# Optimization experiments

Measured on AMD Instinct MI355X. Metric: run time of the kernel, lower is better.

Reference implementation:

```python
import jax, jax.numpy as jnp
import numpy as np

D_MODEL = 1024
NUM_HEADS = 16
D_K = D_MODEL // NUM_HEADS
LN_EPS = 1e-5


def setup_inputs() -> dict:
    key = jax.random.key(0)
    ks = jax.random.split(key, 9)
    s = 1.0 / np.sqrt(D_MODEL)
    x = jax.random.normal(ks[0], (4, 2048, D_MODEL), dtype=jnp.float32)
    Wq = jax.random.uniform(ks[1], (D_MODEL, D_MODEL), minval=-s, maxval=s, dtype=jnp.float32)
    bq = jax.random.uniform(ks[2], (D_MODEL,), minval=-s, maxval=s, dtype=jnp.float32)
    Wk = jax.random.uniform(ks[3], (D_MODEL, D_MODEL), minval=-s, maxval=s, dtype=jnp.float32)
    bk = jax.random.uniform(ks[4], (D_MODEL,), minval=-s, maxval=s, dtype=jnp.float32)
    Wv = jax.random.uniform(ks[5], (D_MODEL, D_MODEL), minval=-s, maxval=s, dtype=jnp.float32)
    bv = jax.random.uniform(ks[6], (D_MODEL,), minval=-s, maxval=s, dtype=jnp.float32)
    Wo = jax.random.uniform(ks[7], (D_MODEL, D_MODEL), minval=-s, maxval=s, dtype=jnp.float32)
    bo = jax.random.uniform(ks[8], (D_MODEL,), minval=-s, maxval=s, dtype=jnp.float32)
    gamma = jnp.ones((D_MODEL,), dtype=jnp.float32)
    beta = jnp.zeros((D_MODEL,), dtype=jnp.float32)
    return {"x": x, "Wq": Wq, "bq": bq, "Wk": Wk, "bk": bk, "Wv": Wv, "bv": bv,
            "Wo": Wo, "bo": bo, "gamma": gamma, "beta": beta}


def reference(x, Wq, bq, Wk, bk, Wv, bv, Wo, bo, gamma, beta):
    B, S, D = x.shape
    H, dk = NUM_HEADS, D_K
    # torch Linear: y = x @ W^T + b; split heads -> (B, H, S, dk)
    def proj(W, b):
        return (jnp.einsum('bsd,ed->bse', x, W) + b).reshape(B, S, H, dk).transpose(0, 2, 1, 3)
    Q = proj(Wq, bq)
    K = proj(Wk, bk)
    V = proj(Wv, bv)
    scores = jnp.einsum('bhqd,bhkd->bhqk', Q, K) / jnp.sqrt(jnp.float32(dk))
    attn = jax.nn.softmax(scores, axis=-1)  # dropout is identity in eval mode
    ctx = jnp.einsum('bhqk,bhkd->bhqd', attn, V)
    ctx = ctx.transpose(0, 2, 1, 3).reshape(B, S, D)
    out = jnp.einsum('bsd,ed->bse', ctx, Wo) + bo
    y = out + x
    mu = jnp.mean(y, axis=-1, keepdims=True)
    var = jnp.mean(jnp.square(y - mu), axis=-1, keepdims=True)
    return (y - mu) * jax.lax.rsqrt(var + LN_EPS) * gamma + beta
```

## Files before the change

### kernel.cpp

```cpp
#include <hip/hip_runtime.h>


#define SEQ 2048
#define DMODEL 1024
#define NH 16
#define DK 64
#define NROWS 8192

typedef unsigned short u16;
typedef unsigned int u32;
typedef __bf16 bf16;
typedef bf16 bf16x8 __attribute__((ext_vector_type(8)));
typedef float f32x4 __attribute__((ext_vector_type(4)));
typedef float f32x16 __attribute__((ext_vector_type(16)));
typedef unsigned u32x2 __attribute__((ext_vector_type(2)));

__device__ inline u16 bfbits(float f) { return __builtin_bit_cast(u16, (bf16)f); }
__device__ inline u32 packbf2(float a, float b) {
    return (u32)bfbits(a) | ((u32)bfbits(b) << 16);
}

__device__ inline float sexp2(float s) {
    return __builtin_bit_cast(float, (u32)(int)fmaf(s, 8388608.0f, 1064986823.0f));
}

__device__ inline void gload16(const u16* g, u16* l) {
    __builtin_amdgcn_global_load_lds(
        (const __attribute__((address_space(1))) u32*)g,
        (__attribute__((address_space(3))) u32*)l, 16, 0, 0);
}

__device__ inline void plswap(u32& a, u32& b) {
#if __has_builtin(__builtin_amdgcn_permlane32_swap)
    u32x2 r = __builtin_amdgcn_permlane32_swap(a, b, false, false);
    a = r[0]; b = r[1];
#else
    u32 xa = __shfl_xor(a, 32), xb = __shfl_xor(b, 32);
    int hi = (threadIdx.x & 63) >> 5;
    u32 na = hi ? xb : a;
    u32 nb = hi ? b : xa;
    a = na; b = nb;
#endif
}

__global__ __launch_bounds__(256) void cvt_f32_bf16(const float* __restrict__ in,
                                                    u16* __restrict__ out, int n) {
    int i = (blockIdx.x * 256 + threadIdx.x) * 4;
    if (i >= n) return;
    float4 v = *(const float4*)(in + i);
    ushort4 o;
    o.x = bfbits(v.x); o.y = bfbits(v.y); o.z = bfbits(v.z); o.w = bfbits(v.w);
    *(ushort4*)(out + i) = o;
}

__global__ __launch_bounds__(256) void cvt4_w(const float* __restrict__ w0,
                                              const float* __restrict__ w1,
                                              const float* __restrict__ w2,
                                              const float* __restrict__ w3,
                                              u16* __restrict__ o0, u16* __restrict__ o1,
                                              u16* __restrict__ o2, u16* __restrict__ o3) {
    const float* in;
    u16* out;
    switch (blockIdx.y) {
        case 0: in = w0; out = o0; break;
        case 1: in = w1; out = o1; break;
        case 2: in = w2; out = o2; break;
        default: in = w3; out = o3; break;
    }
    int i = (blockIdx.x * 256 + threadIdx.x) * 4;
    float4 v = *(const float4*)(in + i);
    ushort4 o;
    o.x = bfbits(v.x); o.y = bfbits(v.y); o.z = bfbits(v.z); o.w = bfbits(v.w);
    *(ushort4*)(out + i) = o;
}

template <int EPI>
__global__ __launch_bounds__(256) void gemm_bt(
    const u16* __restrict__ A, const u16* __restrict__ Bm,
    const float* __restrict__ bias0, const float* __restrict__ bias1,
    const float* __restrict__ bias2,
    u16* __restrict__ Qo, u16* __restrict__ Ko, u16* __restrict__ Vo,
    const float* __restrict__ xres, float* __restrict__ yout) {
    __shared__ __align__(16) u16 smem[16384];
    u16* As = smem;
    u16* Bs = smem + 8192;

    const int tid  = threadIdx.x;
    const int lane = tid & 63;
    const int w    = tid >> 6;
    const int wr   = (w >> 1) * 64;
    const int wc   = (w & 1) * 64;
    const int l16  = lane & 15;
    const int lq   = lane >> 4;
    const int m0   = blockIdx.x * 128;
    const int n0   = blockIdx.y * 128;

    f32x4 acc[4][4];
#pragma unroll
    for (int m = 0; m < 4; m++)
#pragma unroll
        for (int n = 0; n < 4; n++) {
            f32x4 z = {0.f, 0.f, 0.f, 0.f};
            acc[m][n] = z;
        }

    const int l8r = lane >> 3;
    const int sch = (lane & 7) ^ l8r;
    const u16* a_g = A  + (size_t)(m0 + w * 32 + l8r) * 1024 + sch * 8;
    const u16* b_g = Bm + (size_t)(n0 + w * 32 + l8r) * 1024 + sch * 8;

    for (int k0 = 0; k0 < 1024; k0 += 64) {
        __syncthreads();
#pragma unroll
        for (int i = 0; i < 4; i++) {
            gload16(a_g + (size_t)i * 8192 + k0, As + (w * 32 + i * 8) * 64);
            gload16(b_g + (size_t)i * 8192 + k0, Bs + (w * 32 + i * 8) * 64);
        }
        __syncthreads();

#pragma unroll
        for (int kk = 0; kk < 2; kk++) {
            bf16x8 af[4], bfr[4];
#pragma unroll
            for (int m = 0; m < 4; m++)
                af[m] = *(const bf16x8*)&As[(wr + m * 16 + l16) * 64 +
                                            (((kk << 2) | lq) ^ (l16 & 7)) * 8];
#pragma unroll
            for (int n = 0; n < 4; n++)
                bfr[n] = *(const bf16x8*)&Bs[(wc + n * 16 + l16) * 64 +
                                             (((kk << 2) | lq) ^ (l16 & 7)) * 8];
            __builtin_amdgcn_s_setprio(1);
#pragma unroll
            for (int m = 0; m < 4; m++)
#pragma unroll
                for (int n = 0; n < 4; n++)
                    acc[m][n] = __builtin_amdgcn_mfma_f32_16x16x32_bf16(
                        af[m], bfr[n], acc[m][n], 0, 0, 0);
            __builtin_amdgcn_s_setprio(0);
        }
    }

    if (EPI == 0 && n0 >= 2048) {
        const int e0 = n0 - 2048;
        __syncthreads();
#pragma unroll
        for (int m = 0; m < 4; m++)
#pragma unroll
            for (int n = 0; n < 4; n++) {
                const int col = wc + n * 16 + l16;
                const int row = wr + lq * 4 + m * 16;
                const float bias = bias2[e0 + col];
                ushort4 pk;
                pk.x = bfbits(acc[m][n][0] + bias);
                pk.y = bfbits(acc[m][n][1] + bias);
                pk.z = bfbits(acc[m][n][2] + bias);
                pk.w = bfbits(acc[m][n][3] + bias);
                *(ushort4*)&smem[col * 128 + (row ^ ((col & 7) << 3))] = pk;
            }
        __syncthreads();
        const int b = m0 >> 11;
        const int sbase = m0 & 2047;
#pragma unroll
        for (int i = 0; i < 8; i++) {
            const int c = tid + 256 * i;
            const int col = c >> 4;
            const int s0 = (c & 15) * 8;
            uint4 val = *(const uint4*)&smem[col * 128 + (s0 ^ ((col & 7) << 3))];
            const int eg = e0 + col;
            const int bh = b * NH + (eg >> 6);
            *(uint4*)&Vo[((size_t)bh * DK + (eg & 63)) * SEQ + sbase + s0] = val;
        }
        return;
    }

    const int rbase = m0 + wr + lq * 4;
    const int cbase = n0 + wc + l16;
#pragma unroll
    for (int m = 0; m < 4; m++)
#pragma unroll
        for (int n = 0; n < 4; n++) {
            const int col = cbase + n * 16;
#pragma unroll
            for (int r = 0; r < 4; r++) {
                const int row = rbase + m * 16 + r;
                float v = acc[m][n][r];
                if (EPI == 0) {
                    const int which = col >> 10;
                    const int e = col & 1023;
                    v += (which == 0) ? bias0[e] : bias1[e];
                    if (which == 0) v *= 0.18033688011112042f;
                    const int h = e >> 6, d = e & 63;
                    const int b = row >> 11, s = row & 2047;
                    const int bh = b * NH + h;
                    if (which == 0)
                        Qo[((size_t)bh * SEQ + s) * DK + d] = bfbits(v);
                    else
                        Ko[((size_t)bh * SEQ + s) * DK + d] = bfbits(v);
                } else {
                    v += bias0[col] + xres[(size_t)row * DMODEL + col];
                    yout[(size_t)row * DMODEL + col] = v;
                }
            }
        }
}

__global__ __launch_bounds__(512) void attn(const u16* __restrict__ Qb,
                                            const u16* __restrict__ Kb,
                                            const u16* __restrict__ Vtb,
                                            u16* __restrict__ ctx) {
    __shared__ __align__(16) u16 smem[16384];

    const int tid  = threadIdx.x;
    const int lane = tid & 63;
    const int w    = tid >> 6;
    const int q    = lane & 31;
    const int hi   = lane >> 5;
    const int bh   = blockIdx.x;
    const int q0   = blockIdx.y * 256 + w * 32;

    const u16* qp = Qb + ((size_t)bh * SEQ + q0 + q) * DK + hi * 8;
    bf16x8 qf0 = *(const bf16x8*)(qp);
    bf16x8 qf1 = *(const bf16x8*)(qp + 16);
    bf16x8 qf2 = *(const bf16x8*)(qp + 32);
    bf16x8 qf3 = *(const bf16x8*)(qp + 48);

    const int l8r = lane >> 3;
    const int sch = (lane & 7) ^ l8r;
    const u16* kg = Kb  + ((size_t)bh * SEQ + w * 8 + l8r) * 64 + sch * 8;
    const u16* vg = Vtb + ((size_t)bh * DK  + w * 8 + l8r) * SEQ + sch * 8;
    u16* kl = smem + w * 512;
    u16* vl = smem + 8192 + w * 512;

    f32x16 oacc0, oacc1;
#pragma unroll
    for (int r = 0; r < 16; r++) { oacc0[r] = 0.f; oacc1[r] = 0.f; }
    f32x16 fzero;
#pragma unroll
    for (int r = 0; r < 16; r++) fzero[r] = 0.f;
    float l_ = 0.f;

    gload16(kg, kl);
    gload16(vg, vl);
    __syncthreads();

    for (int t = 0; t < SEQ / 64; t++) {
        if (t < SEQ / 64 - 1) {
            gload16(kg + (size_t)(t + 1) * 4096, kl + ((t + 1) & 1) * 4096);
            gload16(vg + (size_t)(t + 1) * 64,  vl + ((t + 1) & 1) * 4096);
        }
        const u16* Kl = smem + (t & 1) * 4096;
        const u16* Vl = smem + 8192 + (t & 1) * 4096;

        f32x16 sacc0, sacc1;
        {
            bf16x8 k00 = *(const bf16x8*)&Kl[(q)      * 64 + ((0 | hi) ^ (q & 7)) * 8];
            bf16x8 k01 = *(const bf16x8*)&Kl[(q)      * 64 + ((2 | hi) ^ (q & 7)) * 8];
            bf16x8 k02 = *(const bf16x8*)&Kl[(q)      * 64 + ((4 | hi) ^ (q & 7)) * 8];
            bf16x8 k03 = *(const bf16x8*)&Kl[(q)      * 64 + ((6 | hi) ^ (q & 7)) * 8];
            bf16x8 k10 = *(const bf16x8*)&Kl[(q + 32) * 64 + ((0 | hi) ^ (q & 7)) * 8];
            bf16x8 k11 = *(const bf16x8*)&Kl[(q + 32) * 64 + ((2 | hi) ^ (q & 7)) * 8];
            bf16x8 k12 = *(const bf16x8*)&Kl[(q + 32) * 64 + ((4 | hi) ^ (q & 7)) * 8];
            bf16x8 k13 = *(const bf16x8*)&Kl[(q + 32) * 64 + ((6 | hi) ^ (q & 7)) * 8];
            __builtin_amdgcn_s_setprio(1);
            sacc0 = __builtin_amdgcn_mfma_f32_32x32x16_bf16(k00, qf0, fzero, 0, 0, 0);
            sacc1 = __builtin_amdgcn_mfma_f32_32x32x16_bf16(k10, qf0, fzero, 0, 0, 0);
            sacc0 = __builtin_amdgcn_mfma_f32_32x32x16_bf16(k01, qf1, sacc0, 0, 0, 0);
            sacc1 = __builtin_amdgcn_mfma_f32_32x32x16_bf16(k11, qf1, sacc1, 0, 0, 0);
            sacc0 = __builtin_amdgcn_mfma_f32_32x32x16_bf16(k02, qf2, sacc0, 0, 0, 0);
            sacc1 = __builtin_amdgcn_mfma_f32_32x32x16_bf16(k12, qf2, sacc1, 0, 0, 0);
            sacc0 = __builtin_amdgcn_mfma_f32_32x32x16_bf16(k03, qf3, sacc0, 0, 0, 0);
            sacc1 = __builtin_amdgcn_mfma_f32_32x32x16_bf16(k13, qf3, sacc1, 0, 0, 0);
            __builtin_amdgcn_s_setprio(0);
        }

#pragma unroll
        for (int r = 0; r < 16; r++) sacc0[r] = sexp2(sacc0[r]);
#pragma unroll
        for (int r = 0; r < 16; r++) sacc1[r] = sexp2(sacc1[r]);
        {
            float s0 = ((sacc0[0] + sacc0[1]) + (sacc0[2] + sacc0[3])) +
                       ((sacc0[4] + sacc0[5]) + (sacc0[6] + sacc0[7]));
            float s1 = ((sacc0[8] + sacc0[9]) + (sacc0[10] + sacc0[11])) +
                       ((sacc0[12] + sacc0[13]) + (sacc0[14] + sacc0[15]));
            float s2 = ((sacc1[0] + sacc1[1]) + (sacc1[2] + sacc1[3])) +
                       ((sacc1[4] + sacc1[5]) + (sacc1[6] + sacc1[7]));
            float s3 = ((sacc1[8] + sacc1[9]) + (sacc1[10] + sacc1[11])) +
                       ((sacc1[12] + sacc1[13]) + (sacc1[14] + sacc1[15]));
            l_ += (s0 + s1) + (s2 + s3);
        }

        u32 wa[8], wb[8];
#pragma unroll
        for (int i = 0; i < 8; i++) wa[i] = packbf2(sacc0[2 * i], sacc0[2 * i + 1]);
#pragma unroll
        for (int i = 0; i < 8; i++) wb[i] = packbf2(sacc1[2 * i], sacc1[2 * i + 1]);
        plswap(wa[0], wa[2]); plswap(wa[1], wa[3]);
        plswap(wa[4], wa[6]); plswap(wa[5], wa[7]);
        plswap(wb[0], wb[2]); plswap(wb[1], wb[3]);
        plswap(wb[4], wb[6]); plswap(wb[5], wb[7]);
        union { u32 u[4]; bf16x8 v; } pf0, pf1, pf2, pf3;
        pf0.u[0] = wa[0]; pf0.u[1] = wa[1]; pf0.u[2] = wa[2]; pf0.u[3] = wa[3];
        pf1.u[0] = wa[4]; pf1.u[1] = wa[5]; pf1.u[2] = wa[6]; pf1.u[3] = wa[7];
        pf2.u[0] = wb[0]; pf2.u[1] = wb[1]; pf2.u[2] = wb[2]; pf2.u[3] = wb[3];
        pf3.u[0] = wb[4]; pf3.u[1] = wb[5]; pf3.u[2] = wb[6]; pf3.u[3] = wb[7];

        {
            bf16x8 v00 = *(const bf16x8*)&Vl[(q)      * 64 + ((0 | hi) ^ (q & 7)) * 8];
            bf16x8 v01 = *(const bf16x8*)&Vl[(q)      * 64 + ((2 | hi) ^ (q & 7)) * 8];
            bf16x8 v02 = *(const bf16x8*)&Vl[(q)      * 64 + ((4 | hi) ^ (q & 7)) * 8];
            bf16x8 v03 = *(const bf16x8*)&Vl[(q)      * 64 + ((6 | hi) ^ (q & 7)) * 8];
            bf16x8 v10 = *(const bf16x8*)&Vl[(q + 32) * 64 + ((0 | hi) ^ (q & 7)) * 8];
            bf16x8 v11 = *(const bf16x8*)&Vl[(q + 32) * 64 + ((2 | hi) ^ (q & 7)) * 8];
            bf16x8 v12 = *(const bf16x8*)&Vl[(q + 32) * 64 + ((4 | hi) ^ (q & 7)) * 8];
            bf16x8 v13 = *(const bf16x8*)&Vl[(q + 32) * 64 + ((6 | hi) ^ (q & 7)) * 8];
            __builtin_amdgcn_s_setprio(1);
            oacc0 = __builtin_amdgcn_mfma_f32_32x32x16_bf16(v00, pf0.v, oacc0, 0, 0, 0);
            oacc1 = __builtin_amdgcn_mfma_f32_32x32x16_bf16(v10, pf0.v, oacc1, 0, 0, 0);
            oacc0 = __builtin_amdgcn_mfma_f32_32x32x16_bf16(v01, pf1.v, oacc0, 0, 0, 0);
            oacc1 = __builtin_amdgcn_mfma_f32_32x32x16_bf16(v11, pf1.v, oacc1, 0, 0, 0);
            oacc0 = __builtin_amdgcn_mfma_f32_32x32x16_bf16(v02, pf2.v, oacc0, 0, 0, 0);
            oacc1 = __builtin_amdgcn_mfma_f32_32x32x16_bf16(v12, pf2.v, oacc1, 0, 0, 0);
            oacc0 = __builtin_amdgcn_mfma_f32_32x32x16_bf16(v03, pf3.v, oacc0, 0, 0, 0);
            oacc1 = __builtin_amdgcn_mfma_f32_32x32x16_bf16(v13, pf3.v, oacc1, 0, 0, 0);
            __builtin_amdgcn_s_setprio(0);
        }

        __syncthreads();
    }

    const float lfull = l_ + __shfl_xor(l_, 32);
    const float invl = 1.f / lfull;
    const int wbase = w * 2048;
#pragma unroll
    for (int r = 0; r < 16; r++) {
        const int dk0 = (r & 3) + 8 * (r >> 2) + 4 * hi;
        const int dk1 = 32 + dk0;
        smem[wbase + q * 64 + (((dk0 >> 3) ^ (q & 7)) << 3) + (dk0 & 7)] = bfbits(oacc0[r] * invl);
        smem[wbase + q * 64 + (((dk1 >> 3) ^ (q & 7)) << 3) + (dk1 & 7)] = bfbits(oacc1[r] * invl);
    }
    __syncthreads();
    const int b = bh >> 4, h = bh & 15;
    const int r4 = lane >> 1;
    const int cc = (lane & 1) * 4;
#pragma unroll
    for (int c = 0; c < 4; c++) {
        const int chunk = cc + c;
        uint4 val = *(const uint4*)&smem[wbase + r4 * 64 + ((chunk ^ (r4 & 7)) << 3)];
        *(uint4*)&ctx[((size_t)(b * SEQ + q0 + r4)) * DMODEL + h * DK + chunk * 8] = val;
    }
}

__global__ __launch_bounds__(256) void ln_inplace(float* __restrict__ y,
                                                  const float* __restrict__ gamma,
                                                  const float* __restrict__ beta) {
    const int row = blockIdx.x;
    float* p = y + (size_t)row * DMODEL;
    const int tid = threadIdx.x;
    float4 v = *(const float4*)(p + tid * 4);
    float s  = v.x + v.y + v.z + v.w;
    float sq = v.x * v.x + v.y * v.y + v.z * v.z + v.w * v.w;
#pragma unroll
    for (int m = 1; m < 64; m <<= 1) {
        s  += __shfl_xor(s, m);
        sq += __shfl_xor(sq, m);
    }
    __shared__ float rs[4], rq[4];
    if ((tid & 63) == 0) { rs[tid >> 6] = s; rq[tid >> 6] = sq; }
    __syncthreads();
    s  = rs[0] + rs[1] + rs[2] + rs[3];
    sq = rq[0] + rq[1] + rq[2] + rq[3];
    const float mean = s * (1.0f / 1024.0f);
    const float var  = sq * (1.0f / 1024.0f) - mean * mean;
    const float inv  = rsqrtf(var + 1e-5f);
    const int c = tid * 4;
    float4 g4 = *(const float4*)(gamma + c);
    float4 b4 = *(const float4*)(beta + c);
    float4 o;
    o.x = (v.x - mean) * inv * g4.x + b4.x;
    o.y = (v.y - mean) * inv * g4.y + b4.y;
    o.z = (v.z - mean) * inv * g4.z + b4.z;
    o.w = (v.w - mean) * inv * g4.w + b4.w;
    *(float4*)(p + c) = o;
}

extern "C" void kernel_launch(void* const* d_in, const int* in_sizes, int n_in,
                              void* d_out, int out_size, void* d_ws, size_t ws_size,
                              hipStream_t stream) {
    const float* x     = (const float*)d_in[0];
    const float* Wq    = (const float*)d_in[1];
    const float* bq    = (const float*)d_in[2];
    const float* Wk    = (const float*)d_in[3];
    const float* bk    = (const float*)d_in[4];
    const float* Wv    = (const float*)d_in[5];
    const float* bv    = (const float*)d_in[6];
    const float* Wo    = (const float*)d_in[7];
    const float* bo    = (const float*)d_in[8];
    const float* gamma = (const float*)d_in[9];
    const float* beta  = (const float*)d_in[10];
    float* out = (float*)d_out;

    u16* x_bf    = (u16*)d_ws;
    u16* Wqkv_bf = x_bf + (size_t)NROWS * DMODEL;
    u16* Wo_bf   = Wqkv_bf + (size_t)3072 * 1024;
    u16* Q_bf    = Wo_bf + (size_t)1024 * 1024;
    u16* K_bf    = Q_bf + (size_t)64 * SEQ * DK;
    u16* Vt_bf   = K_bf + (size_t)64 * SEQ * DK;
    u16* ctx_bf  = x_bf;

    cvt_f32_bf16<<<8192, 256, 0, stream>>>(x, x_bf, NROWS * DMODEL);
    cvt4_w<<<dim3(1024, 4), 256, 0, stream>>>(Wq, Wk, Wv, Wo,
                                              Wqkv_bf, Wqkv_bf + 1048576,
                                              Wqkv_bf + 2097152, Wo_bf);

    gemm_bt<0><<<dim3(64, 24), 256, 0, stream>>>(x_bf, Wqkv_bf,
                                                 bq, bk, bv, Q_bf, K_bf, Vt_bf,
                                                 nullptr, nullptr);
    attn<<<dim3(64, 8), 512, 0, stream>>>(Q_bf, K_bf, Vt_bf, ctx_bf);
    gemm_bt<1><<<dim3(64, 8), 256, 0, stream>>>(ctx_bf, Wo_bf,
                                                bo, nullptr, nullptr,
                                                nullptr, nullptr, nullptr,
                                                x, out);
    ln_inplace<<<8192, 256, 0, stream>>>(out, gamma, beta);
}
```

Baseline: 204.6 us.

## Split attention over two key halves and add a combine kernel

```diff
diff --git a/kernel.cpp b/kernel.cpp
--- a/kernel.cpp
+++ b/kernel.cpp
@@ -18,6 +18,9 @@
 __device__ inline u16 bfbits(float f) { return __builtin_bit_cast(u16, (bf16)f); }
 __device__ inline u32 packbf2(float a, float b) {
     return (u32)bfbits(a) | ((u32)bfbits(b) << 16);
+}
+__device__ inline float bf2f(u16 h) {
+    union { u32 u; float f; } v; v.u = (u32)h << 16; return v.f;
 }
 
 __device__ inline float sexp2(float s) {
@@ -207,7 +210,8 @@
 __global__ __launch_bounds__(512) void attn(const u16* __restrict__ Qb,
                                             const u16* __restrict__ Kb,
                                             const u16* __restrict__ Vtb,
-                                            u16* __restrict__ ctx) {
+                                            u16* __restrict__ pO,
+                                            float* __restrict__ lG) {
     __shared__ __align__(16) u16 smem[16384];
 
     const int tid  = threadIdx.x;
@@ -216,6 +220,7 @@
     const int q    = lane & 31;
     const int hi   = lane >> 5;
     const int bh   = blockIdx.x;
+    const int ks   = blockIdx.z;
     const int q0   = blockIdx.y * 256 + w * 32;
 
     const u16* qp = Qb + ((size_t)bh * SEQ + q0 + q) * DK + hi * 8;
@@ -226,8 +231,8 @@
 
     const int l8r = lane >> 3;
     const int sch = (lane & 7) ^ l8r;
-    const u16* kg = Kb  + ((size_t)bh * SEQ + w * 8 + l8r) * 64 + sch * 8;
-    const u16* vg = Vtb + ((size_t)bh * DK  + w * 8 + l8r) * SEQ + sch * 8;
+    const u16* kg = Kb  + ((size_t)bh * SEQ + ks * 1024 + w * 8 + l8r) * 64 + sch * 8;
+    const u16* vg = Vtb + ((size_t)bh * DK + w * 8 + l8r) * SEQ + ks * 1024 + sch * 8;
     u16* kl = smem + w * 512;
     u16* vl = smem + 8192 + w * 512;
 
@@ -243,8 +248,8 @@
     gload16(vg, vl);
     __syncthreads();
 
-    for (int t = 0; t < SEQ / 64; t++) {
-        if (t < SEQ / 64 - 1) {
+    for (int t = 0; t < 16; t++) {
+        if (t < 15) {
             gload16(kg + (size_t)(t + 1) * 4096, kl + ((t + 1) & 1) * 4096);
             gload16(vg + (size_t)(t + 1) * 64,  vl + ((t + 1) & 1) * 4096);
         }
@@ -328,26 +333,44 @@
         __syncthreads();
     }
 
-    const float lfull = l_ + __shfl_xor(l_, 32);
-    const float invl = 1.f / lfull;
+    l_ = l_ + __shfl_xor(l_, 32);
+    if (lane < 32) lG[((size_t)(ks * 64 + bh)) * SEQ + q0 + lane] = l_;
+
     const int wbase = w * 2048;
 #pragma unroll
     for (int r = 0; r < 16; r++) {
         const int dk0 = (r & 3) + 8 * (r >> 2) + 4 * hi;
         const int dk1 = 32 + dk0;
-        smem[wbase + q * 64 + (((dk0 >> 3) ^ (q & 7)) << 3) + (dk0 & 7)] = bfbits(oacc0[r] * invl);
-        smem[wbase + q * 64 + (((dk1 >> 3) ^ (q & 7)) << 3) + (dk1 & 7)] = bfbits(oacc1[r] * invl);
+        smem[wbase + q * 64 + (((dk0 >> 3) ^ (q & 7)) << 3) + (dk0 & 7)] = bfbits(oacc0[r]);
+        smem[wbase + q * 64 + (((dk1 >> 3) ^ (q & 7)) << 3) + (dk1 & 7)] = bfbits(oacc1[r]);
     }
     __syncthreads();
-    const int b = bh >> 4, h = bh & 15;
     const int r4 = lane >> 1;
     const int cc = (lane & 1) * 4;
 #pragma unroll
     for (int c = 0; c < 4; c++) {
         const int chunk = cc + c;
         uint4 val = *(const uint4*)&smem[wbase + r4 * 64 + ((chunk ^ (r4 & 7)) << 3)];
-        *(uint4*)&ctx[((size_t)(b * SEQ + q0 + r4)) * DMODEL + h * DK + chunk * 8] = val;
-    }
+        *(uint4*)&pO[(((size_t)(ks * 64 + bh)) * SEQ + q0 + r4) * DK + chunk * 8] = val;
+    }
+}
+
+__global__ __launch_bounds__(256) void combine(const u16* __restrict__ pO,
+                                               const float* __restrict__ lG,
+                                               u16* __restrict__ ctx) {
+    const int t = blockIdx.x * 256 + threadIdx.x;
+    const int chunk = t & 7;
+    const int s = (t >> 3) & 2047;
+    const int bh = t >> 14;
+    const float inv = 1.f / (lG[(size_t)bh * SEQ + s] + lG[(size_t)(64 + bh) * SEQ + s]);
+    union { uint4 v; u16 h[8]; } a, b, o;
+    a.v = *(const uint4*)&pO[((size_t)bh * SEQ + s) * DK + chunk * 8];
+    b.v = *(const uint4*)&pO[((size_t)(64 + bh) * SEQ + s) * DK + chunk * 8];
+#pragma unroll
+    for (int i = 0; i < 8; i++)
+        o.h[i] = bfbits((bf2f(a.h[i]) + bf2f(b.h[i])) * inv);
+    const int bb = bh >> 4, h = bh & 15;
+    *(uint4*)&ctx[((size_t)(bb * SEQ + s)) * DMODEL + h * DK + chunk * 8] = o.v;
 }
 
 __global__ __launch_bounds__(256) void ln_inplace(float* __restrict__ y,
@@ -406,6 +429,8 @@
     u16* K_bf    = Q_bf + (size_t)64 * SEQ * DK;
     u16* Vt_bf   = K_bf + (size_t)64 * SEQ * DK;
     u16* ctx_bf  = x_bf;
+    u16* pO      = (u16*)d_out;
+    float* lG    = (float*)Wqkv_bf;
 
     cvt_f32_bf16<<<8192, 256, 0, stream>>>(x, x_bf, NROWS * DMODEL);
     cvt4_w<<<dim3(1024, 4), 256, 0, stream>>>(Wq, Wk, Wv, Wo,
@@ -415,7 +440,8 @@
     gemm_bt<0><<<dim3(64, 24), 256, 0, stream>>>(x_bf, Wqkv_bf,
                                                  bq, bk, bv, Q_bf, K_bf, Vt_bf,
                                                  nullptr, nullptr);
-    attn<<<dim3(64, 8), 512, 0, stream>>>(Q_bf, K_bf, Vt_bf, ctx_bf);
+    attn<<<dim3(64, 8, 2), 512, 0, stream>>>(Q_bf, K_bf, Vt_bf, pO, lG);
+    combine<<<4096, 256, 0, stream>>>(pO, lG, ctx_bf);
     gemm_bt<1><<<dim3(64, 8), 256, 0, stream>>>(ctx_bf, Wo_bf,
                                                 bo, nullptr, nullptr,
                                                 nullptr, nullptr, nullptr,
```

After: 217.0 us. 1.06x slower.

## Merge conversion kernels and split attention tile loop to cut register pressure

Applied to the files above, without the earlier changes.

```diff
diff --git a/kernel.cpp b/kernel.cpp
--- a/kernel.cpp
+++ b/kernel.cpp
@@ -43,31 +43,29 @@
 #endif
 }
 
-__global__ __launch_bounds__(256) void cvt_f32_bf16(const float* __restrict__ in,
-                                                    u16* __restrict__ out, int n) {
-    int i = (blockIdx.x * 256 + threadIdx.x) * 4;
-    if (i >= n) return;
-    float4 v = *(const float4*)(in + i);
-    ushort4 o;
-    o.x = bfbits(v.x); o.y = bfbits(v.y); o.z = bfbits(v.z); o.w = bfbits(v.w);
-    *(ushort4*)(out + i) = o;
-}
-
-__global__ __launch_bounds__(256) void cvt4_w(const float* __restrict__ w0,
-                                              const float* __restrict__ w1,
-                                              const float* __restrict__ w2,
-                                              const float* __restrict__ w3,
-                                              u16* __restrict__ o0, u16* __restrict__ o1,
-                                              u16* __restrict__ o2, u16* __restrict__ o3) {
+__global__ __launch_bounds__(256) void cvt_all(
+    const float* __restrict__ x,  const float* __restrict__ w0,
+    const float* __restrict__ w1, const float* __restrict__ w2,
+    const float* __restrict__ w3,
+    u16* __restrict__ xo, u16* __restrict__ o0, u16* __restrict__ o1,
+    u16* __restrict__ o2, u16* __restrict__ o3) {
+    const int b = blockIdx.x;
     const float* in;
     u16* out;
-    switch (blockIdx.y) {
-        case 0: in = w0; out = o0; break;
-        case 1: in = w1; out = o1; break;
-        case 2: in = w2; out = o2; break;
-        default: in = w3; out = o3; break;
-    }
-    int i = (blockIdx.x * 256 + threadIdx.x) * 4;
+    int base;
+    if (b < 8192) {
+        in = x; out = xo; base = b << 10;
+    } else {
+        const int wsel = (b - 8192) >> 10;
+        base = ((b - 8192) & 1023) << 10;
+        switch (wsel) {
+            case 0: in = w0; out = o0; break;
+            case 1: in = w1; out = o1; break;
+            case 2: in = w2; out = o2; break;
+            default: in = w3; out = o3; break;
+        }
+    }
+    const int i = base + threadIdx.x * 4;
     float4 v = *(const float4*)(in + i);
     ushort4 o;
     o.x = bfbits(v.x); o.y = bfbits(v.y); o.z = bfbits(v.z); o.w = bfbits(v.w);
@@ -204,10 +202,10 @@
         }
 }
 
-__global__ __launch_bounds__(512) void attn(const u16* __restrict__ Qb,
-                                            const u16* __restrict__ Kb,
-                                            const u16* __restrict__ Vtb,
-                                            u16* __restrict__ ctx) {
+__global__ __launch_bounds__(512, 4) void attn(const u16* __restrict__ Qb,
+                                               const u16* __restrict__ Kb,
+                                               const u16* __restrict__ Vtb,
+                                               u16* __restrict__ ctx) {
     __shared__ __align__(16) u16 smem[16384];
 
     const int tid  = threadIdx.x;
@@ -251,77 +249,50 @@
         const u16* Kl = smem + (t & 1) * 4096;
         const u16* Vl = smem + 8192 + (t & 1) * 4096;
 
-        f32x16 sacc0, sacc1;
-        {
-            bf16x8 k00 = *(const bf16x8*)&Kl[(q)      * 64 + ((0 | hi) ^ (q & 7)) * 8];
-            bf16x8 k01 = *(const bf16x8*)&Kl[(q)      * 64 + ((2 | hi) ^ (q & 7)) * 8];
-            bf16x8 k02 = *(const bf16x8*)&Kl[(q)      * 64 + ((4 | hi) ^ (q & 7)) * 8];
-            bf16x8 k03 = *(const bf16x8*)&Kl[(q)      * 64 + ((6 | hi) ^ (q & 7)) * 8];
-            bf16x8 k10 = *(const bf16x8*)&Kl[(q + 32) * 64 + ((0 | hi) ^ (q & 7)) * 8];
-            bf16x8 k11 = *(const bf16x8*)&Kl[(q + 32) * 64 + ((2 | hi) ^ (q & 7)) * 8];
-            bf16x8 k12 = *(const bf16x8*)&Kl[(q + 32) * 64 + ((4 | hi) ^ (q & 7)) * 8];
-            bf16x8 k13 = *(const bf16x8*)&Kl[(q + 32) * 64 + ((6 | hi) ^ (q & 7)) * 8];
+#pragma unroll
+        for (int half = 0; half < 2; half++) {
+            const int kr = q + half * 32;
+            bf16x8 ka = *(const bf16x8*)&Kl[kr * 64 + ((0 | hi) ^ (q & 7)) * 8];
+            bf16x8 kb = *(const bf16x8*)&Kl[kr * 64 + ((2 | hi) ^ (q & 7)) * 8];
+            bf16x8 kc = *(const bf16x8*)&Kl[kr * 64 + ((4 | hi) ^ (q & 7)) * 8];
+            bf16x8 kd = *(const bf16x8*)&Kl[kr * 64 + ((6 | hi) ^ (q & 7)) * 8];
             __builtin_amdgcn_s_setprio(1);
-            sacc0 = __builtin_amdgcn_mfma_f32_32x32x16_bf16(k00, qf0, fzero, 0, 0, 0);
-            sacc1 = __builtin_amdgcn_mfma_f32_32x32x16_bf16(k10, qf0, fzero, 0, 0, 0);
-            sacc0 = __builtin_amdgcn_mfma_f32_32x32x16_bf16(k01, qf1, sacc0, 0, 0, 0);
-            sacc1 = __builtin_amdgcn_mfma_f32_32x32x16_bf16(k11, qf1, sacc1, 0, 0, 0);
-            sacc0 = __builtin_amdgcn_mfma_f32_32x32x16_bf16(k02, qf2, sacc0, 0, 0, 0);
-            sacc1 = __builtin_amdgcn_mfma_f32_32x32x16_bf16(k12, qf2, sacc1, 0, 0, 0);
-            sacc0 = __builtin_amdgcn_mfma_f32_32x32x16_bf16(k03, qf3, sacc0, 0, 0, 0);
-            sacc1 = __builtin_amdgcn_mfma_f32_32x32x16_bf16(k13, qf3, sacc1, 0, 0, 0);
+            f32x16 sacc = __builtin_amdgcn_mfma_f32_32x32x16_bf16(ka, qf0, fzero, 0, 0, 0);
+            sacc = __builtin_amdgcn_mfma_f32_32x32x16_bf16(kb, qf1, sacc, 0, 0, 0);
+            sacc = __builtin_amdgcn_mfma_f32_32x32x16_bf16(kc, qf2, sacc, 0, 0, 0);
+            sacc = __builtin_amdgcn_mfma_f32_32x32x16_bf16(kd, qf3, sacc, 0, 0, 0);
             __builtin_amdgcn_s_setprio(0);
-        }
-
-#pragma unroll
-        for (int r = 0; r < 16; r++) sacc0[r] = sexp2(sacc0[r]);
-#pragma unroll
-        for (int r = 0; r < 16; r++) sacc1[r] = sexp2(sacc1[r]);
-        {
-            float s0 = ((sacc0[0] + sacc0[1]) + (sacc0[2] + sacc0[3])) +
-                       ((sacc0[4] + sacc0[5]) + (sacc0[6] + sacc0[7]));
-            float s1 = ((sacc0[8] + sacc0[9]) + (sacc0[10] + sacc0[11])) +
-                       ((sacc0[12] + sacc0[13]) + (sacc0[14] + sacc0[15]));
-            float s2 = ((sacc1[0] + sacc1[1]) + (sacc1[2] + sacc1[3])) +
-                       ((sacc1[4] + sacc1[5]) + (sacc1[6] + sacc1[7]));
-            float s3 = ((sacc1[8] + sacc1[9]) + (sacc1[10] + sacc1[11])) +
-                       ((sacc1[12] + sacc1[13]) + (sacc1[14] + sacc1[15]));
-            l_ += (s0 + s1) + (s2 + s3);
-        }
-
-        u32 wa[8], wb[8];
-#pragma unroll
-        for (int i = 0; i < 8; i++) wa[i] = packbf2(sacc0[2 * i], sacc0[2 * i + 1]);
-#pragma unroll
-        for (int i = 0; i < 8; i++) wb[i] = packbf2(sacc1[2 * i], sacc1[2 * i + 1]);
-        plswap(wa[0], wa[2]); plswap(wa[1], wa[3]);
-        plswap(wa[4], wa[6]); plswap(wa[5], wa[7]);
-        plswap(wb[0], wb[2]); plswap(wb[1], wb[3]);
-        plswap(wb[4], wb[6]); plswap(wb[5], wb[7]);
-        union { u32 u[4]; bf16x8 v; } pf0, pf1, pf2, pf3;
-        pf0.u[0] = wa[0]; pf0.u[1] = wa[1]; pf0.u[2] = wa[2]; pf0.u[3] = wa[3];
-        pf1.u[0] = wa[4]; pf1.u[1] = wa[5]; pf1.u[2] = wa[6]; pf1.u[3] = wa[7];
-        pf2.u[0] = wb[0]; pf2.u[1] = wb[1]; pf2.u[2] = wb[2]; pf2.u[3] = wb[3];
-        pf3.u[0] = wb[4]; pf3.u[1] = wb[5]; pf3.u[2] = wb[6]; pf3.u[3] = wb[7];
-
-        {
-            bf16x8 v00 = *(const bf16x8*)&Vl[(q)      * 64 + ((0 | hi) ^ (q & 7)) * 8];
-            bf16x8 v01 = *(const bf16x8*)&Vl[(q)      * 64 + ((2 | hi) ^ (q & 7)) * 8];
-            bf16x8 v02 = *(const bf16x8*)&Vl[(q)      * 64 + ((4 | hi) ^ (q & 7)) * 8];
-            bf16x8 v03 = *(const bf16x8*)&Vl[(q)      * 64 + ((6 | hi) ^ (q & 7)) * 8];
-            bf16x8 v10 = *(const bf16x8*)&Vl[(q + 32) * 64 + ((0 | hi) ^ (q & 7)) * 8];
-            bf16x8 v11 = *(const bf16x8*)&Vl[(q + 32) * 64 + ((2 | hi) ^ (q & 7)) * 8];
-            bf16x8 v12 = *(const bf16x8*)&Vl[(q + 32) * 64 + ((4 | hi) ^ (q & 7)) * 8];
-            bf16x8 v13 = *(const bf16x8*)&Vl[(q + 32) * 64 + ((6 | hi) ^ (q & 7)) * 8];
+
+#pragma unroll
+            for (int r = 0; r < 16; r++) sacc[r] = sexp2(sacc[r]);
+            {
+                float s0 = ((sacc[0] + sacc[1]) + (sacc[2] + sacc[3])) +
+                           ((sacc[4] + sacc[5]) + (sacc[6] + sacc[7]));
+                float s1 = ((sacc[8] + sacc[9]) + (sacc[10] + sacc[11])) +
+                           ((sacc[12] + sacc[13]) + (sacc[14] + sacc[15]));
+                l_ += s0 + s1;
+            }
+
+            u32 wa[8];
+#pragma unroll
+            for (int i = 0; i < 8; i++) wa[i] = packbf2(sacc[2 * i], sacc[2 * i + 1]);
+            plswap(wa[0], wa[2]); plswap(wa[1], wa[3]);
+            plswap(wa[4], wa[6]); plswap(wa[5], wa[7]);
+            union { u32 u[4]; bf16x8 v; } pf0, pf1;
+            pf0.u[0] = wa[0]; pf0.u[1] = wa[1]; pf0.u[2] = wa[2]; pf0.u[3] = wa[3];
+            pf1.u[0] = wa[4]; pf1.u[1] = wa[5]; pf1.u[2] = wa[6]; pf1.u[3] = wa[7];
+
+            const int c0 = ((half * 2 + 0) * 2) | hi;
+            const int c1 = ((half * 2 + 1) * 2) | hi;
+            bf16x8 va = *(const bf16x8*)&Vl[(q)      * 64 + (c0 ^ (q & 7)) * 8];
+            bf16x8 vb = *(const bf16x8*)&Vl[(q)      * 64 + (c1 ^ (q & 7)) * 8];
+            bf16x8 vc = *(const bf16x8*)&Vl[(q + 32) * 64 + (c0 ^ (q & 7)) * 8];
+            bf16x8 vd = *(const bf16x8*)&Vl[(q + 32) * 64 + (c1 ^ (q & 7)) * 8];
             __builtin_amdgcn_s_setprio(1);
-            oacc0 = __builtin_amdgcn_mfma_f32_32x32x16_bf16(v00, pf0.v, oacc0, 0, 0, 0);
-            oacc1 = __builtin_amdgcn_mfma_f32_32x32x16_bf16(v10, pf0.v, oacc1, 0, 0, 0);
-            oacc0 = __builtin_amdgcn_mfma_f32_32x32x16_bf16(v01, pf1.v, oacc0, 0, 0, 0);
-            oacc1 = __builtin_amdgcn_mfma_f32_32x32x16_bf16(v11, pf1.v, oacc1, 0, 0, 0);
-            oacc0 = __builtin_amdgcn_mfma_f32_32x32x16_bf16(v02, pf2.v, oacc0, 0, 0, 0);
-            oacc1 = __builtin_amdgcn_mfma_f32_32x32x16_bf16(v12, pf2.v, oacc1, 0, 0, 0);
-            oacc0 = __builtin_amdgcn_mfma_f32_32x32x16_bf16(v03, pf3.v, oacc0, 0, 0, 0);
-            oacc1 = __builtin_amdgcn_mfma_f32_32x32x16_bf16(v13, pf3.v, oacc1, 0, 0, 0);
+            oacc0 = __builtin_amdgcn_mfma_f32_32x32x16_bf16(va, pf0.v, oacc0, 0, 0, 0);
+            oacc1 = __builtin_amdgcn_mfma_f32_32x32x16_bf16(vc, pf0.v, oacc1, 0, 0, 0);
+            oacc0 = __builtin_amdgcn_mfma_f32_32x32x16_bf16(vb, pf1.v, oacc0, 0, 0, 0);
+            oacc1 = __builtin_amdgcn_mfma_f32_32x32x16_bf16(vd, pf1.v, oacc1, 0, 0, 0);
             __builtin_amdgcn_s_setprio(0);
         }
 
@@ -407,10 +378,9 @@
     u16* Vt_bf   = K_bf + (size_t)64 * SEQ * DK;
     u16* ctx_bf  = x_bf;
 
-    cvt_f32_bf16<<<8192, 256, 0, stream>>>(x, x_bf, NROWS * DMODEL);
-    cvt4_w<<<dim3(1024, 4), 256, 0, stream>>>(Wq, Wk, Wv, Wo,
-                                              Wqkv_bf, Wqkv_bf + 1048576,
-                                              Wqkv_bf + 2097152, Wo_bf);
+    cvt_all<<<12288, 256, 0, stream>>>(x, Wq, Wk, Wv, Wo,
+                                       x_bf, Wqkv_bf, Wqkv_bf + 1048576,
+                                       Wqkv_bf + 2097152, Wo_bf);
 
     gemm_bt<0><<<dim3(64, 24), 256, 0, stream>>>(x_bf, Wqkv_bf,
                                                  bq, bk, bv, Q_bf, K_bf, Vt_bf,
```

Measured after the change: 204.7 us. No clear change (+0.0%).

## Double-buffer QKV GEMM with 128x256 tiles and merge conversion kernels

Applied to the files above, without the earlier changes.

```diff
diff --git a/kernel.cpp b/kernel.cpp
--- a/kernel.cpp
+++ b/kernel.cpp
@@ -43,57 +43,51 @@
 #endif
 }
 
-__global__ __launch_bounds__(256) void cvt_f32_bf16(const float* __restrict__ in,
-                                                    u16* __restrict__ out, int n) {
-    int i = (blockIdx.x * 256 + threadIdx.x) * 4;
-    if (i >= n) return;
+__global__ __launch_bounds__(256) void cvt_all(
+    const float* __restrict__ x,  const float* __restrict__ w0,
+    const float* __restrict__ w1, const float* __restrict__ w2,
+    const float* __restrict__ w3,
+    u16* __restrict__ xo, u16* __restrict__ o0, u16* __restrict__ o1,
+    u16* __restrict__ o2, u16* __restrict__ o3) {
+    const int b = blockIdx.x;
+    const float* in;
+    u16* out;
+    int base;
+    if (b < 8192) {
+        in = x; out = xo; base = b << 10;
+    } else {
+        const int wsel = (b - 8192) >> 10;
+        base = ((b - 8192) & 1023) << 10;
+        switch (wsel) {
+            case 0: in = w0; out = o0; break;
+            case 1: in = w1; out = o1; break;
+            case 2: in = w2; out = o2; break;
+            default: in = w3; out = o3; break;
+        }
+    }
+    const int i = base + threadIdx.x * 4;
     float4 v = *(const float4*)(in + i);
     ushort4 o;
     o.x = bfbits(v.x); o.y = bfbits(v.y); o.z = bfbits(v.z); o.w = bfbits(v.w);
     *(ushort4*)(out + i) = o;
 }
 
-__global__ __launch_bounds__(256) void cvt4_w(const float* __restrict__ w0,
-                                              const float* __restrict__ w1,
-                                              const float* __restrict__ w2,
-                                              const float* __restrict__ w3,
-                                              u16* __restrict__ o0, u16* __restrict__ o1,
-                                              u16* __restrict__ o2, u16* __restrict__ o3) {
-    const float* in;
-    u16* out;
-    switch (blockIdx.y) {
-        case 0: in = w0; out = o0; break;
-        case 1: in = w1; out = o1; break;
-        case 2: in = w2; out = o2; break;
-        default: in = w3; out = o3; break;
-    }
-    int i = (blockIdx.x * 256 + threadIdx.x) * 4;
-    float4 v = *(const float4*)(in + i);
-    ushort4 o;
-    o.x = bfbits(v.x); o.y = bfbits(v.y); o.z = bfbits(v.z); o.w = bfbits(v.w);
-    *(ushort4*)(out + i) = o;
-}
-
-template <int EPI>
-__global__ __launch_bounds__(256) void gemm_bt(
+__global__ __launch_bounds__(512) void gemm_qkv(
     const u16* __restrict__ A, const u16* __restrict__ Bm,
-    const float* __restrict__ bias0, const float* __restrict__ bias1,
-    const float* __restrict__ bias2,
-    u16* __restrict__ Qo, u16* __restrict__ Ko, u16* __restrict__ Vo,
-    const float* __restrict__ xres, float* __restrict__ yout) {
-    __shared__ __align__(16) u16 smem[16384];
-    u16* As = smem;
-    u16* Bs = smem + 8192;
+    const float* __restrict__ bq, const float* __restrict__ bk,
+    const float* __restrict__ bv,
+    u16* __restrict__ Qo, u16* __restrict__ Ko, u16* __restrict__ Vo) {
+    __shared__ __align__(16) u16 smem[49152];
 
     const int tid  = threadIdx.x;
     const int lane = tid & 63;
     const int w    = tid >> 6;
-    const int wr   = (w >> 1) * 64;
-    const int wc   = (w & 1) * 64;
+    const int wr   = (w >> 2) * 64;
+    const int wc   = (w & 3) * 64;
     const int l16  = lane & 15;
     const int lq   = lane >> 4;
     const int m0   = blockIdx.x * 128;
-    const int n0   = blockIdx.y * 128;
+    const int n0   = blockIdx.y * 256;
 
     f32x4 acc[4][4];
 #pragma unroll
@@ -106,29 +100,42 @@
 
     const int l8r = lane >> 3;
     const int sch = (lane & 7) ^ l8r;
-    const u16* a_g = A  + (size_t)(m0 + w * 32 + l8r) * 1024 + sch * 8;
-    const u16* b_g = Bm + (size_t)(n0 + w * 32 + l8r) * 1024 + sch * 8;
-
-    for (int k0 = 0; k0 < 1024; k0 += 64) {
-        __syncthreads();
-#pragma unroll
-        for (int i = 0; i < 4; i++) {
-            gload16(a_g + (size_t)i * 8192 + k0, As + (w * 32 + i * 8) * 64);
-            gload16(b_g + (size_t)i * 8192 + k0, Bs + (w * 32 + i * 8) * 64);
-        }
-        __syncthreads();
-
+    const u16* a_g = A  + (size_t)(m0 + w * 8 + l8r) * 1024 + sch * 8;
+    const u16* b_g = Bm + (size_t)(n0 + w * 8 + l8r) * 1024 + sch * 8;
+    u16* asd = smem + (w * 8) * 64;
+    u16* bsd = smem + 16384 + (w * 8) * 64;
+
+#define STAGE(kt, c) do {                                                  \
+        gload16(a_g + (kt) * 64,          asd + (c) * 8192);               \
+        gload16(a_g + 65536 + (kt) * 64,  asd + (c) * 8192 + 4096);        \
+        gload16(b_g + (kt) * 64,          bsd + (c) * 16384);              \
+        gload16(b_g + 65536 + (kt) * 64,  bsd + (c) * 16384 + 4096);       \
+        gload16(b_g + 131072 + (kt) * 64, bsd + (c) * 16384 + 8192);       \
+        gload16(b_g + 196608 + (kt) * 64, bsd + (c) * 16384 + 12288);      \
+    } while (0)
+
+    STAGE(0, 0);
+    STAGE(1, 1);
+
+    for (int kt = 0; kt < 16; kt++) {
+        const int cur = kt & 1;
+        if (kt < 15) asm volatile("s_waitcnt vmcnt(6)" ::: "memory");
+        else         asm volatile("s_waitcnt vmcnt(0)" ::: "memory");
+        __builtin_amdgcn_s_barrier();
+
+        const u16* Asl = smem + cur * 8192;
+        const u16* Bsl = smem + 16384 + cur * 16384;
 #pragma unroll
         for (int kk = 0; kk < 2; kk++) {
             bf16x8 af[4], bfr[4];
 #pragma unroll
             for (int m = 0; m < 4; m++)
-                af[m] = *(const bf16x8*)&As[(wr + m * 16 + l16) * 64 +
-                                            (((kk << 2) | lq) ^ (l16 & 7)) * 8];
+                af[m] = *(const bf16x8*)&Asl[(wr + m * 16 + l16) * 64 +
+                                             (((kk << 2) | lq) ^ (l16 & 7)) * 8];
 #pragma unroll
             for (int n = 0; n < 4; n++)
-                bfr[n] = *(const bf16x8*)&Bs[(wc + n * 16 + l16) * 64 +
-                                             (((kk << 2) | lq) ^ (l16 & 7)) * 8];
+                bfr[n] = *(const bf16x8*)&Bsl[(wc + n * 16 + l16) * 64 +
+                                              (((kk << 2) | lq) ^ (l16 & 7)) * 8];
             __builtin_amdgcn_s_setprio(1);
 #pragma unroll
             for (int m = 0; m < 4; m++)
@@ -138,18 +145,20 @@
                         af[m], bfr[n], acc[m][n], 0, 0, 0);
             __builtin_amdgcn_s_setprio(0);
         }
-    }
-
-    if (EPI == 0 && n0 >= 2048) {
+        __builtin_amdgcn_s_barrier();
+        if (kt < 14) STAGE(kt + 2, cur);
+    }
+#undef STAGE
+
+    if (n0 >= 2048) {
         const int e0 = n0 - 2048;
-        __syncthreads();
 #pragma unroll
         for (int m = 0; m < 4; m++)
 #pragma unroll
             for (int n = 0; n < 4; n++) {
                 const int col = wc + n * 16 + l16;
                 const int row = wr + lq * 4 + m * 16;
-                const float bias = bias2[e0 + col];
+                const float bias = bv[e0 + col];
                 ushort4 pk;
                 pk.x = bfbits(acc[m][n][0] + bias);
                 pk.y = bfbits(acc[m][n][1] + bias);
@@ -162,7 +171,7 @@
         const int sbase = m0 & 2047;
 #pragma unroll
         for (int i = 0; i < 8; i++) {
-            const int c = tid + 256 * i;
+            const int c = tid + 512 * i;
             const int col = c >> 4;
             const int s0 = (c & 15) * 8;
             uint4 val = *(const uint4*)&smem[col * 128 + (s0 ^ ((col & 7) << 3))];
@@ -173,6 +182,93 @@
         return;
     }
 
+    const int which = n0 >> 10;
+    const int rbase = m0 + wr + lq * 4;
+#pragma unroll
+    for (int m = 0; m < 4; m++)
+#pragma unroll
+        for (int n = 0; n < 4; n++) {
+            const int e = ((n0 & 1023) + wc + n * 16 + l16);
+            const float bias = (which == 0) ? bq[e] : bk[e];
+            const int h = e >> 6, d = e & 63;
+#pragma unroll
+            for (int r = 0; r < 4; r++) {
+                const int row = rbase + m * 16 + r;
+                float v = acc[m][n][r] + bias;
+                if (which == 0) v *= 0.18033688011112042f;
+                const int b = row >> 11, s = row & 2047;
+                const int bh = b * NH + h;
+                if (which == 0)
+                    Qo[((size_t)bh * SEQ + s) * DK + d] = bfbits(v);
+                else
+                    Ko[((size_t)bh * SEQ + s) * DK + d] = bfbits(v);
+            }
+        }
+}
+
+__global__ __launch_bounds__(256) void gemm_o(
+    const u16* __restrict__ A, const u16* __restrict__ Bm,
+    const float* __restrict__ bias,
+    const float* __restrict__ xres, float* __restrict__ yout) {
+    __shared__ __align__(16) u16 smem[16384];
+    u16* As = smem;
+    u16* Bs = smem + 8192;
+
+    const int tid  = threadIdx.x;
+    const int lane = tid & 63;
+    const int w    = tid >> 6;
+    const int wr   = (w >> 1) * 64;
+    const int wc   = (w & 1) * 64;
+    const int l16  = lane & 15;
+    const int lq   = lane >> 4;
+    const int m0   = blockIdx.x * 128;
+    const int n0   = blockIdx.y * 128;
+
+    f32x4 acc[4][4];
+#pragma unroll
+    for (int m = 0; m < 4; m++)
+#pragma unroll
+        for (int n = 0; n < 4; n++) {
+            f32x4 z = {0.f, 0.f, 0.f, 0.f};
+            acc[m][n] = z;
+        }
+
+    const int l8r = lane >> 3;
+    const int sch = (lane & 7) ^ l8r;
+    const u16* a_g = A  + (size_t)(m0 + w * 32 + l8r) * 1024 + sch * 8;
+    const u16* b_g = Bm + (size_t)(n0 + w * 32 + l8r) * 1024 + sch * 8;
+
+    for (int k0 = 0; k0 < 1024; k0 += 64) {
+        __syncthreads();
+#pragma unroll
+        for (int i = 0; i < 4; i++) {
+            gload16(a_g + (size_t)i * 8192 + k0, As + (w * 32 + i * 8) * 64);
+            gload16(b_g + (size_t)i * 8192 + k0, Bs + (w * 32 + i * 8) * 64);
+        }
+        __syncthreads();
+
+#pragma unroll
+        for (int kk = 0; kk < 2; kk++) {
+            bf16x8 af[4], bfr[4];
+#pragma unroll
+            for (int m = 0; m < 4; m++)
+                af[m] = *(const bf16x8*)&As[(wr + m * 16 + l16) * 64 +
+                                            (((kk << 2) | lq) ^ (l16 & 7)) * 8];
+#pragma unroll
+            for (int n = 0; n < 4; n++)
+                bfr[n] = *(const bf16x8*)&Bs[(wc + n * 16 + l16) * 64 +
+                                             (((kk << 2) | lq) ^ (l16 & 7)) * 8];
+            __builtin_amdgcn_s_setprio(1);
+#pragma unroll
+            for (int m = 0; m < 4; m++)
+#pragma unroll
+                for (int n = 0; n < 4; n++)
+                    acc[m][n] = __builtin_amdgcn_mfma_f32_16x16x32_bf16(
+                        af[m], bfr[n], acc[m][n], 0, 0, 0);
+            __builtin_amdgcn_s_setprio(0);
+        }
+    }
+
     const int rbase = m0 + wr + lq * 4;
     const int cbase = n0 + wc + l16;
 #pragma unroll
@@ -183,23 +279,8 @@
 #pragma unroll
             for (int r = 0; r < 4; r++) {
                 const int row = rbase + m * 16 + r;
-                float v = acc[m][n][r];
-                if (EPI == 0) {
-                    const int which = col >> 10;
-                    const int e = col & 1023;
-                    v += (which == 0) ? bias0[e] : bias1[e];
-                    if (which == 0) v *= 0.18033688011112042f;
-                    const int h = e >> 6, d = e & 63;
-                    const int b = row >> 11, s = row & 2047;
-                    const int bh = b * NH + h;
-                    if (which == 0)
-                        Qo[((size_t)bh * SEQ + s) * DK + d] = bfbits(v);
-                    else
-                        Ko[((size_t)bh * SEQ + s) * DK + d] = bfbits(v);
-                } else {
-                    v += bias0[col] + xres[(size_t)row * DMODEL + col];
-                    yout[(size_t)row * DMODEL + col] = v;
-                }
+                float v = acc[m][n][r] + bias[col] + xres[(size_t)row * DMODEL + col];
+                yout[(size_t)row * DMODEL + col] = v;
             }
         }
 }
@@ -407,18 +488,13 @@
     u16* Vt_bf   = K_bf + (size_t)64 * SEQ * DK;
     u16* ctx_bf  = x_bf;
 
-    cvt_f32_bf16<<<8192, 256, 0, stream>>>(x, x_bf, NROWS * DMODEL);
-    cvt4_w<<<dim3(1024, 4), 256, 0, stream>>>(Wq, Wk, Wv, Wo,
-                                              Wqkv_bf, Wqkv_bf + 1048576,
-                                              Wqkv_bf + 2097152, Wo_bf);
-
-    gemm_bt<0><<<dim3(64, 24), 256, 0, stream>>>(x_bf, Wqkv_bf,
-                                                 bq, bk, bv, Q_bf, K_bf, Vt_bf,
-                                                 nullptr, nullptr);
+    cvt_all<<<12288, 256, 0, stream>>>(x, Wq, Wk, Wv, Wo,
+                                       x_bf, Wqkv_bf, Wqkv_bf + 1048576,
+                                       Wqkv_bf + 2097152, Wo_bf);
+
+    gemm_qkv<<<dim3(64, 12), 512, 0, stream>>>(x_bf, Wqkv_bf,
+                                               bq, bk, bv, Q_bf, K_bf, Vt_bf);
     attn<<<dim3(64, 8), 512, 0, stream>>>(Q_bf, K_bf, Vt_bf, ctx_bf);
-    gemm_bt<1><<<dim3(64, 8), 256, 0, stream>>>(ctx_bf, Wo_bf,
-                                                bo, nullptr, nullptr,
-                                                nullptr, nullptr, nullptr,
-                                                x, out);
+    gemm_o<<<dim3(64, 8), 256, 0, stream>>>(ctx_bf, Wo_bf, bo, x, out);
     ln_inplace<<<8192, 256, 0, stream>>>(out, gamma, beta);
 }
```

Measured after the change: 200.1 us. 2.2% less time.
